# Kernel optimization log

Measured on AMD Instinct MI355X. Metric: run time of the kernel, lower is better.

Reference implementation:

```python
import jax, jax.numpy as jnp
import numpy as np

K = 1024  # codebook size
D = 256   # code dim
B, L = 32, 1024  # batch, tokens


def setup_inputs() -> dict:
    key = jax.random.key(0)
    k1, k2 = jax.random.split(key)
    z_e_x = jax.random.normal(k1, (B, L, D), dtype=jnp.float32)
    # nn.Embedding weight init: uniform(-1/K, 1/K)
    embedding = jax.random.uniform(k2, (K, D), dtype=jnp.float32,
                                   minval=-1.0 / K, maxval=1.0 / K)
    return {"z_e_x": z_e_x, "embedding": embedding}


def reference(z_e_x, embedding):
    # vq(): nearest-neighbor codebook lookup -> integer indices, shape z_e_x.shape[:-1]
    flat = z_e_x.reshape(-1, z_e_x.shape[-1])                      # [N, D]
    # squared L2 distances via expansion: ||z||^2 - 2 z.e + ||e||^2
    d = (jnp.sum(flat * flat, axis=1, keepdims=True)
         - 2.0 * flat @ embedding.T
         + jnp.sum(embedding * embedding, axis=1))                 # [N, K]
    idx = jnp.argmin(d, axis=1)                                    # [N]
    return idx.reshape(z_e_x.shape[:-1])
```

## Files before the change

### kernel.cpp

```cpp
#include <hip/hip_runtime.h>


#define DDIM 256
#define KCODES 1024
#define TAU 1.6e-4f
#define WIN 1.2e-4f
#define LISTCAP 16384
#define CANDCAP 16
#define P2GRID 2048

typedef __attribute__((ext_vector_type(8))) _Float16 f16x8;
typedef __attribute__((ext_vector_type(2))) _Float16 h2;
typedef __attribute__((ext_vector_type(4))) float f32x4;
typedef __attribute__((ext_vector_type(8))) unsigned short u16x8;

__device__ __forceinline__ float block128_sq(const float* __restrict__ a)
{
#pragma clang fp contract(off)
    float r[8];
    #pragma unroll
    for (int j = 0; j < 8; ++j) { float v = a[j]; r[j] = v * v; }
    #pragma unroll
    for (int i = 8; i < 128; i += 8) {
        #pragma unroll
        for (int j = 0; j < 8; ++j) { float v = a[i + j]; r[j] = r[j] + v * v; }
    }
    return ((r[0] + r[1]) + (r[2] + r[3])) + ((r[4] + r[5]) + (r[6] + r[7]));
}

__global__ __launch_bounds__(256) void vq_prep(
    const float* __restrict__ emb, unsigned short* __restrict__ e16,
    float* __restrict__ s2, int* __restrict__ count)
{
    const int tid = threadIdx.x;
    if (blockIdx.x == 0 && tid == 0) *count = 0;

    const int id = blockIdx.x * 256 + tid;
    const float* src = emb + (size_t)id * 8;
    float4 p0 = *reinterpret_cast<const float4*>(src);
    float4 p1 = *reinterpret_cast<const float4*>(src + 4);
    float fv[8] = {p0.x, p0.y, p0.z, p0.w, p1.x, p1.y, p1.z, p1.w};
    u16x8 vh;
    #pragma unroll
    for (int e = 0; e < 8; ++e) {
        _Float16 h = (_Float16)(fv[e] * 1024.0f);
        vh[e] = __builtin_bit_cast(unsigned short, h);
    }
    *reinterpret_cast<u16x8*>(e16 + (size_t)id * 8) = vh;

    if (tid < 8) {
        const int c = blockIdx.x * 8 + tid;
        const float* e = emb + (size_t)c * DDIM;
        s2[c] = block128_sq(e) + block128_sq(e + 128);
    }
}

__global__ __launch_bounds__(512, 2) void vq_pass1(
    const float* __restrict__ z, const unsigned short* __restrict__ e16,
    const float* __restrict__ s2g, int* __restrict__ out,
    int* __restrict__ count, int* __restrict__ list, int N)
{
    __shared__ __align__(16) unsigned short Bt[2][32768];
    __shared__ float s2s[KCODES];

    const int tid  = threadIdx.x;
    const int wid  = tid >> 6, lane = tid & 63;
    const int ll   = lane & 15, lg = lane >> 4;
    const int rowbase = blockIdx.x * 128 + wid * 16;

    for (int c = tid; c < KCODES; c += 512) s2s[c] = s2g[c];

    const int sB     = (ll >> 1) & 3;
    const int rdbase = ll * 32 + ((lg ^ sB) << 3);

    f16x8 afrag[8];
    #pragma unroll
    for (int ks = 0; ks < 8; ++ks) {
        const float* zp = z + (size_t)(rowbase + ll) * DDIM + ks * 32 + lg * 8;
        float4 p0 = *reinterpret_cast<const float4*>(zp);
        float4 p1 = *reinterpret_cast<const float4*>(zp + 4);
        float fv[8] = {p0.x, p0.y, p0.z, p0.w, p1.x, p1.y, p1.z, p1.w};
        #pragma unroll
        for (int e = 0; e < 8; ++e) afrag[ks][e] = (_Float16)fv[e];
    }

    #define STAGE(ct_, buf_)                                                      \
        {                                                                         \
            const int ct_v = (ct_);                                               \
            _Pragma("unroll")                                                     \
            for (int q = 0; q < 8; ++q) {                                         \
                int id = q * 512 + tid;                                           \
                int ks = id >> 9, rem = id & 511, cl = rem >> 2, pc = rem & 3;    \
                int clog = pc ^ ((cl >> 1) & 3);                                  \
                const unsigned short* src = e16 +                                 \
                    (size_t)(ct_v * 128 + cl) * DDIM + ks * 32 + clog * 8;        \
                __builtin_amdgcn_global_load_lds(                                 \
                    (const __attribute__((address_space(1))) void*)src,           \
                    (__attribute__((address_space(3))) void*)&Bt[buf_][(size_t)id * 8], \
                    16, 0, 0);                                                    \
            }                                                                     \
        }

    float bv[4], sv[4];
    int   bk[4];
    #pragma unroll
    for (int j = 0; j < 4; ++j) { bv[j] = 3.4e38f; sv[j] = 3.4e38f; bk[j] = 0; }

    STAGE(0, 0);

    for (int ct = 0; ct < 8; ++ct) {
        const int buf = ct & 1;
        __syncthreads();

        if (ct < 7) STAGE(ct + 1, buf ^ 1);

        f32x4 acc[8];
        const f32x4 zero4 = {0.f, 0.f, 0.f, 0.f};
        #pragma unroll
        for (int n = 0; n < 8; ++n) acc[n] = zero4;

        #pragma unroll
        for (int ks = 0; ks < 8; ++ks) {
            #pragma unroll
            for (int n = 0; n < 8; ++n) {
                f16x8 bh = *reinterpret_cast<const f16x8*>(
                    &Bt[buf][ks * 4096 + n * 512 + rdbase]);
                acc[n] = __builtin_amdgcn_mfma_f32_16x16x32_f16(
                    afrag[ks], bh, acc[n], 0, 0, 0);
            }
        }

        #pragma unroll
        for (int n = 0; n < 8; ++n) {
            const int c = ct * 128 + n * 16 + ll;
            const float s2v = s2s[c];
            #pragma unroll
            for (int j = 0; j < 4; ++j) {
                float v = fmaf(-0.001953125f, acc[n][j], s2v);
                if (v < bv[j] || (v == bv[j] && c < bk[j])) {
                    sv[j] = bv[j]; bv[j] = v; bk[j] = c;
                } else {
                    sv[j] = fminf(sv[j], v);
                }
            }
        }
    }
    #undef STAGE

    #pragma unroll
    for (int off = 1; off < 16; off <<= 1) {
        #pragma unroll
        for (int j = 0; j < 4; ++j) {
            float ob = __shfl_xor(bv[j], off, 64);
            int   ok = __shfl_xor(bk[j], off, 64);
            float os = __shfl_xor(sv[j], off, 64);
            if (ob < bv[j] || (ob == bv[j] && ok < bk[j])) {
                sv[j] = fminf(bv[j], os); bv[j] = ob; bk[j] = ok;
            } else {
                sv[j] = fminf(sv[j], ob);
            }
        }
    }

    if (ll == 0) {
        #pragma unroll
        for (int j = 0; j < 4; ++j) {
            int r = rowbase + lg * 4 + j;
            if (r < N) {
                out[r] = bk[j];
                if (sv[j] - bv[j] <= TAU) {
                    int pos = atomicAdd(count, 1);
                    if (pos < LISTCAP) list[pos] = r;
                }
            }
        }
    }
}

__global__ __launch_bounds__(256, 4) void vq_pass2(
    const float* __restrict__ z, const float* __restrict__ emb,
    const unsigned short* __restrict__ e16, const float* __restrict__ s2g,
    const int* __restrict__ count, const int* __restrict__ list,
    int* __restrict__ out)
{
#pragma clang fp contract(off)
    __shared__ __align__(16) float zls[DDIM];
    __shared__ float vls[KCODES];
    __shared__ float s2s[KCODES];
    __shared__ float s1sh, bvsh;
    __shared__ float wmin[4];
    __shared__ int   candc[CANDCAP];
    __shared__ float cand_v[CANDCAP];
    __shared__ int   ncand;

    const int tid  = threadIdx.x;
    const int wv   = tid >> 6, lane = tid & 63;
    const int cslot = lane >> 2;
    const int sub   = lane & 3;

    int cnt = *count; if (cnt > LISTCAP) cnt = LISTCAP;
    if ((int)blockIdx.x >= cnt) return;

    for (int c = tid; c < KCODES; c += 256) s2s[c] = s2g[c];

    for (int idx = blockIdx.x; idx < cnt; idx += P2GRID) {
        const int row = list[idx];

        if (tid < 64)
            *reinterpret_cast<float4*>(&zls[tid * 4]) =
                *reinterpret_cast<const float4*>(z + (size_t)row * DDIM + tid * 4);
        if (tid == 65) ncand = 0;
        __syncthreads();

        if (tid == 0) s1sh = block128_sq(zls) + block128_sq(zls + 128);

        h2 z16[32];
        {
            const float2* zp2 = reinterpret_cast<const float2*>(&zls[0]);
            #pragma unroll
            for (int q = 0; q < 8; ++q)
                #pragma unroll
                for (int j = 0; j < 4; ++j) {
                    float2 f = zp2[q * 16 + sub * 4 + j];
                    h2 a; a[0] = (_Float16)f.x; a[1] = (_Float16)f.y;
                    z16[q * 4 + j] = a;
                }
        }

        #pragma unroll 1
        for (int i = 0; i < 16; ++i) {
            const int c = wv * 256 + i * 16 + cslot;
            const unsigned short* base = e16 + (size_t)c * DDIM;

            float p = 0.f;
            #pragma unroll
            for (int h = 0; h < 2; ++h) {
                f16x8 e0 = *reinterpret_cast<const f16x8*>(base + (4 * h + 0) * 32 + sub * 8);
                f16x8 e1 = *reinterpret_cast<const f16x8*>(base + (4 * h + 1) * 32 + sub * 8);
                f16x8 e2 = *reinterpret_cast<const f16x8*>(base + (4 * h + 2) * 32 + sub * 8);
                f16x8 e3 = *reinterpret_cast<const f16x8*>(base + (4 * h + 3) * 32 + sub * 8);
                #pragma unroll
                for (int j = 0; j < 4; ++j) {
                    h2 a0; a0[0] = e0[2 * j]; a0[1] = e0[2 * j + 1];
                    h2 a1; a1[0] = e1[2 * j]; a1[1] = e1[2 * j + 1];
                    h2 a2; a2[0] = e2[2 * j]; a2[1] = e2[2 * j + 1];
                    h2 a3; a3[0] = e3[2 * j]; a3[1] = e3[2 * j + 1];
#if __has_builtin(__builtin_amdgcn_fdot2)
                    p = __builtin_amdgcn_fdot2(a0, z16[(4 * h + 0) * 4 + j], p, false);
                    p = __builtin_amdgcn_fdot2(a1, z16[(4 * h + 1) * 4 + j], p, false);
                    p = __builtin_amdgcn_fdot2(a2, z16[(4 * h + 2) * 4 + j], p, false);
                    p = __builtin_amdgcn_fdot2(a3, z16[(4 * h + 3) * 4 + j], p, false);
#else
                    p = fmaf((float)a0[0], (float)z16[(4 * h + 0) * 4 + j][0], p);
                    p = fmaf((float)a0[1], (float)z16[(4 * h + 0) * 4 + j][1], p);
                    p = fmaf((float)a1[0], (float)z16[(4 * h + 1) * 4 + j][0], p);
                    p = fmaf((float)a1[1], (float)z16[(4 * h + 1) * 4 + j][1], p);
                    p = fmaf((float)a2[0], (float)z16[(4 * h + 2) * 4 + j][0], p);
                    p = fmaf((float)a2[1], (float)z16[(4 * h + 2) * 4 + j][1], p);
                    p = fmaf((float)a3[0], (float)z16[(4 * h + 3) * 4 + j][0], p);
                    p = fmaf((float)a3[1], (float)z16[(4 * h + 3) * 4 + j][1], p);
#endif
                }
            }
            p += __shfl_xor(p, 1, 64);
            p += __shfl_xor(p, 2, 64);
            if (sub == 0)
                vls[c] = fmaf(-0.001953125f, p, s2s[c]);
        }
        __syncthreads();

        float m = 3.4e38f;
        #pragma unroll
        for (int k = 0; k < 4; ++k) m = fminf(m, vls[tid + 256 * k]);
        #pragma unroll
        for (int off = 1; off < 64; off <<= 1) m = fminf(m, __shfl_xor(m, off, 64));
        if (lane == 0) wmin[wv] = m;
        __syncthreads();
        if (tid == 0)
            bvsh = fminf(fminf(wmin[0], wmin[1]), fminf(wmin[2], wmin[3]));
        __syncthreads();

        const float thr = bvsh + WIN;
        #pragma unroll
        for (int k = 0; k < 4; ++k) {
            int c = tid + 256 * k;
            if (vls[c] <= thr) {
                int p = atomicAdd(&ncand, 1);
                if (p < CANDCAP) candc[p] = c;
            }
        }
        __syncthreads();
        int nc2 = ncand; if (nc2 > CANDCAP) nc2 = CANDCAP;
        const float s1 = s1sh;

        for (int i = wv; i < nc2; i += 4) {
            const int c = candc[i];
            float4 ev4 = *reinterpret_cast<const float4*>(emb + (size_t)c * DDIM + lane * 4);
            const float* zq = &zls[lane * 4];
            double ds = (double)zq[0] * (double)ev4.x;
            ds = fma((double)zq[1], (double)ev4.y, ds);
            ds = fma((double)zq[2], (double)ev4.z, ds);
            ds = fma((double)zq[3], (double)ev4.w, ds);
            #pragma unroll
            for (int off = 1; off < 64; off <<= 1)
                ds += __shfl_xor(ds, off, 64);
            if (lane == 0) {
                float twog = 2.0f * (float)ds;
                float t1   = s1 - twog;
                cand_v[i]  = t1 + s2s[c];
            }
        }
        __syncthreads();

        if (tid == 0) {
            float bb = 3.4e38f; int kb = KCODES - 1;
            for (int i = 0; i < nc2; ++i) {
                float dv = cand_v[i]; int c = candc[i];
                if (dv < bb || (dv == bb && c < kb)) { bb = dv; kb = c; }
            }
            out[row] = kb;
        }
        __syncthreads();
    }
}

extern "C" void kernel_launch(void* const* d_in, const int* in_sizes, int n_in,
                              void* d_out, int out_size, void* d_ws, size_t ws_size,
                              hipStream_t stream) {
    const float* z   = (const float*)d_in[0];
    const float* emb = (const float*)d_in[1];
    int*   out   = (int*)d_out;
    float* s2    = (float*)d_ws;
    int*   count = (int*)((char*)d_ws + 4096);
    int*   list  = (int*)((char*)d_ws + 4224);
    unsigned short* e16 = (unsigned short*)((char*)d_ws + 131072);
    const int N = in_sizes[0] / DDIM;

    vq_prep<<<dim3(128), dim3(256), 0, stream>>>(emb, e16, s2, count);
    vq_pass1<<<dim3(N / 128), dim3(512), 0, stream>>>(z, e16, s2, out, count, list, N);
    vq_pass2<<<dim3(P2GRID), dim3(256), 0, stream>>>(z, emb, e16, s2, count, list, out);
}
```

Baseline: 72.89 us.

## Shrink pass1 tiles to 32 rows and split codebook across waves

Pass1 now uses 256-thread blocks covering 32 rows, with the four waves split two by rows and two by codebook halves. The B tile in LDS shrinks to a 16 KB double buffer, restaged every k-step instead of every 128-code tile. Partial argmin results from the two code halves are merged through shared memory. The goal is more blocks and higher occupancy (4 per CU, 1024 blocks instead of 256), at the cost of a barrier per k-step and each codebook slice being reloaded by more blocks.

Result: slower. 78.41 us (+7.6%).

```diff
diff --git a/kernel.cpp b/kernel.cpp
--- a/kernel.cpp
+++ b/kernel.cpp
@@ -55,20 +55,24 @@
     }
 }
 
-__global__ __launch_bounds__(512, 2) void vq_pass1(
+__global__ __launch_bounds__(256, 4) void vq_pass1(
     const float* __restrict__ z, const unsigned short* __restrict__ e16,
     const float* __restrict__ s2g, int* __restrict__ out,
     int* __restrict__ count, int* __restrict__ list, int N)
 {
-    __shared__ __align__(16) unsigned short Bt[2][32768];
+    __shared__ __align__(16) unsigned short Bt[2][8192];
     __shared__ float s2s[KCODES];
+    __shared__ float Lbv[2][32], Lsv[2][32];
+    __shared__ int   Lbk[2][32];
 
     const int tid  = threadIdx.x;
     const int wid  = tid >> 6, lane = tid & 63;
     const int ll   = lane & 15, lg = lane >> 4;
-    const int rowbase = blockIdx.x * 128 + wid * 16;
-
-    for (int c = tid; c < KCODES; c += 512) s2s[c] = s2g[c];
+    const int rowHalf  = wid & 1, codeHalf = wid >> 1;
+    const int rowbase  = blockIdx.x * 32 + rowHalf * 16;
+    const int chbase   = codeHalf * 512;
+
+    for (int c = tid; c < KCODES; c += 256) s2s[c] = s2g[c];
 
     const int sB     = (ll >> 1) & 3;
     const int rdbase = ll * 32 + ((lg ^ sB) << 3);
@@ -84,16 +88,17 @@
         for (int e = 0; e < 8; ++e) afrag[ks][e] = (_Float16)fv[e];
     }
 
-    #define STAGE(ct_, buf_)                                                      \
+    #define STAGE(nt_, buf_)                                                      \
         {                                                                         \
-            const int ct_v = (ct_);                                               \
+            const int nt_v = (nt_);                                               \
             _Pragma("unroll")                                                     \
-            for (int q = 0; q < 8; ++q) {                                         \
-                int id = q * 512 + tid;                                           \
-                int ks = id >> 9, rem = id & 511, cl = rem >> 2, pc = rem & 3;    \
+            for (int q = 0; q < 4; ++q) {                                         \
+                int id = q * 256 + tid;                                           \
+                int half = id >> 9, rem = id & 511, cl = rem >> 2, pc = rem & 3;  \
                 int clog = pc ^ ((cl >> 1) & 3);                                  \
                 const unsigned short* src = e16 +                                 \
-                    (size_t)(ct_v * 128 + cl) * DDIM + ks * 32 + clog * 8;        \
+                    (size_t)(half * 512 + (nt_v >> 3) * 128 + cl) * DDIM          \
+                        + (nt_v & 7) * 32 + clog * 8;                             \
                 __builtin_amdgcn_global_load_lds(                                 \
                     (const __attribute__((address_space(1))) void*)src,           \
                     (__attribute__((address_space(3))) void*)&Bt[buf_][(size_t)id * 8], \
@@ -108,12 +113,7 @@
 
     STAGE(0, 0);
 
-    for (int ct = 0; ct < 8; ++ct) {
-        const int buf = ct & 1;
-        __syncthreads();
-
-        if (ct < 7) STAGE(ct + 1, buf ^ 1);
-
+    for (int ct = 0; ct < 4; ++ct) {
         f32x4 acc[8];
         const f32x4 zero4 = {0.f, 0.f, 0.f, 0.f};
         #pragma unroll
@@ -121,10 +121,15 @@
 
         #pragma unroll
         for (int ks = 0; ks < 8; ++ks) {
+            const int t = ct * 8 + ks;
+            __syncthreads();
+
+            if (t < 31) STAGE(t + 1, (t + 1) & 1);
+
+            const unsigned short* bbase = &Bt[t & 1][codeHalf * 4096];
             #pragma unroll
             for (int n = 0; n < 8; ++n) {
-                f16x8 bh = *reinterpret_cast<const f16x8*>(
-                    &Bt[buf][ks * 4096 + n * 512 + rdbase]);
+                f16x8 bh = *reinterpret_cast<const f16x8*>(bbase + n * 512 + rdbase);
                 acc[n] = __builtin_amdgcn_mfma_f32_16x16x32_f16(
                     afrag[ks], bh, acc[n], 0, 0, 0);
             }
@@ -132,7 +137,7 @@
 
         #pragma unroll
         for (int n = 0; n < 8; ++n) {
-            const int c = ct * 128 + n * 16 + ll;
+            const int c = chbase + ct * 128 + n * 16 + ll;
             const float s2v = s2s[c];
             #pragma unroll
             for (int j = 0; j < 4; ++j) {
@@ -165,13 +170,26 @@
     if (ll == 0) {
         #pragma unroll
         for (int j = 0; j < 4; ++j) {
-            int r = rowbase + lg * 4 + j;
-            if (r < N) {
-                out[r] = bk[j];
-                if (sv[j] - bv[j] <= TAU) {
-                    int pos = atomicAdd(count, 1);
-                    if (pos < LISTCAP) list[pos] = r;
-                }
+            int rib = rowHalf * 16 + lg * 4 + j;
+            Lbv[codeHalf][rib] = bv[j];
+            Lsv[codeHalf][rib] = sv[j];
+            Lbk[codeHalf][rib] = bk[j];
+        }
+    }
+    __syncthreads();
+
+    if (tid < 32) {
+        const int r = blockIdx.x * 32 + tid;
+        if (r < N) {
+            float b0 = Lbv[0][tid], s0 = Lsv[0][tid]; int k0 = Lbk[0][tid];
+            float b1 = Lbv[1][tid], s1 = Lsv[1][tid]; int k1 = Lbk[1][tid];
+            float bb, ss; int kk;
+            if (b1 < b0) { bb = b1; kk = k1; ss = fminf(s1, b0); }
+            else         { bb = b0; kk = k0; ss = fminf(s0, b1); }
+            out[r] = kk;
+            if (ss - bb <= TAU) {
+                int pos = atomicAdd(count, 1);
+                if (pos < LISTCAP) list[pos] = r;
             }
         }
     }
@@ -337,6 +355,6 @@
     const int N = in_sizes[0] / DDIM;
 
     vq_prep<<<dim3(128), dim3(256), 0, stream>>>(emb, e16, s2, count);
-    vq_pass1<<<dim3(N / 128), dim3(512), 0, stream>>>(z, e16, s2, out, count, list, N);
+    vq_pass1<<<dim3(N / 32), dim3(256), 0, stream>>>(z, e16, s2, out, count, list, N);
     vq_pass2<<<dim3(P2GRID), dim3(256), 0, stream>>>(z, emb, e16, s2, count, list, out);
 }
```
